# Optimization experiments

Hardware: AMD Instinct MI355X
Metric: run time of the kernel (lower is better)

## Reference

```python
import jax, jax.numpy as jnp
import numpy as np

N_NODES = 65536
N_EDGES = 1048576
IN_F = 128
HID_F = 128
OUT_F = 128


def setup_inputs() -> dict:
    key = jax.random.key(0)
    ks = jax.random.split(key, 8)
    feat = jax.random.normal(ks[0], (N_NODES, IN_F), dtype=jnp.float32)
    eweight = jax.random.uniform(ks[1], (N_EDGES, 1), dtype=jnp.float32)
    W1 = jax.random.normal(ks[2], (IN_F, HID_F), dtype=jnp.float32) * (1.0 / np.sqrt(IN_F))
    b1 = jnp.zeros((HID_F,), dtype=jnp.float32)
    W2 = jax.random.normal(ks[3], (HID_F, OUT_F), dtype=jnp.float32) * (1.0 / np.sqrt(HID_F))
    b2 = jnp.zeros((OUT_F,), dtype=jnp.float32)
    src = jax.random.randint(ks[4], (N_EDGES,), 0, N_NODES, dtype=jnp.int32)
    dst = jax.random.randint(ks[5], (N_EDGES,), 0, N_NODES, dtype=jnp.int32)
    return {"feat": feat, "eweight": eweight, "W1": W1, "b1": b1,
            "W2": W2, "b2": b2, "src": src, "dst": dst}


def _degrees(src, dst, n_nodes):
    ones = jnp.ones(src.shape[0], dtype=jnp.float32)
    deg_out = jax.ops.segment_sum(ones, src, num_segments=n_nodes)
    deg_in = jax.ops.segment_sum(ones, dst, num_segments=n_nodes)
    # DGL GraphConv clamps degree to min 1 before norm='both'
    return jnp.clip(deg_out, 1.0, None), jnp.clip(deg_in, 1.0, None)


def _graph_conv(feat, W, b, src, dst, out_norm, in_norm, n_nodes):
    # DGL GraphConv, norm='both': D_out^{-1/2} x -> x W -> spmm sum -> D_in^{-1/2} -> + b
    h = feat * out_norm[:, None]
    h = h @ W
    agg = jax.ops.segment_sum(h[src], dst, num_segments=n_nodes)
    return agg * in_norm[:, None] + b


def reference(feat, eweight, W1, b1, W2, b2, src, dst):
    n = feat.shape[0]
    deg_out, deg_in = _degrees(src, dst, n)
    out_norm = jax.lax.rsqrt(deg_out)
    in_norm = jax.lax.rsqrt(deg_in)
    h = _graph_conv(feat, W1, b1, src, dst, out_norm, in_norm, n)
    h = jax.nn.relu(h)
    h = _graph_conv(h, W2, b2, src, dst, out_norm, in_norm, n)
    # final update_all: u_mul_e + sum (eweight given)
    msg = h[src] * eweight  # [E, OUT_F]
    return jax.ops.segment_sum(msg, dst, num_segments=n)
```

## Files before the change

kernel.cpp:

```cpp
#include <hip/hip_runtime.h>

#define F 128
#define NBA 512
#define NBS 128
#define COARSE 256
#define CAP_BIN 4864
#define CAP_CSR 5632

typedef unsigned int uint;
typedef unsigned short ushort;
typedef unsigned char uchar;
typedef __attribute__((ext_vector_type(8))) short short8;
typedef __attribute__((ext_vector_type(8))) unsigned short ushort8;
typedef __attribute__((ext_vector_type(4))) float floatx4;

__device__ __forceinline__ ushort f2bf(float f) {
  uint u = __float_as_uint(f);
  u += 0x7fffu + ((u >> 16) & 1u);
  return (ushort)(u >> 16);
}

__global__ __launch_bounds__(256) void w_prep(const float* __restrict__ W1,
                                              const float* __restrict__ W2,
                                              ushort* __restrict__ W1t,
                                              ushort* __restrict__ W2t,
                                              int* __restrict__ cursorD,
                                              int* __restrict__ cursorS) {
  int b = blockIdx.x;
  if (b == 0) cursorD[threadIdx.x] = 0;
  if (b == 1) cursorS[threadIdx.x] = 0;
  const float* W = (b < 64) ? W1 : W2;
  ushort* Wt = (b < 64) ? W1t : W2t;
  int idx = (b & 63) * 256 + threadIdx.x;
  int k = idx >> 7, n = idx & 127;
  Wt[n * F + k] = f2bf(W[idx]);
}

__global__ __launch_bounds__(256) void bin_edges(
    const int* __restrict__ src, const int* __restrict__ dst,
    const float* __restrict__ ew, int E,
    int* __restrict__ cursorD, int* __restrict__ cursorS,
    uint2* __restrict__ slotD, uchar* __restrict__ srcF) {
  __shared__ int cnt[4][COARSE];
  __shared__ int base[COARSE];
  bool isD = blockIdx.x < NBA;
  int blk = isD ? blockIdx.x : blockIdx.x - NBA;
  int nblk = isD ? NBA : NBS;
  const int* key = isD ? dst : src;
  int* cursor = isD ? cursorD : cursorS;
  int wave = threadIdx.x >> 6;
  for (int i = threadIdx.x; i < 4 * COARSE; i += 256) ((int*)cnt)[i] = 0;
  __syncthreads();
  int chunk = (E + nblk - 1) / nblk;
  int s0 = blk * chunk, s1 = min(E, s0 + chunk);
  for (int i = s0 + threadIdx.x; i < s1; i += 256)
    atomicAdd(&cnt[wave][key[i] >> 8], 1);
  __syncthreads();
  if (threadIdx.x < COARSE) {
    int b = threadIdx.x;
    int tot = cnt[0][b] + cnt[1][b] + cnt[2][b] + cnt[3][b];
    base[b] = tot ? atomicAdd(&cursor[b], tot) : 0;
    cnt[0][b] = 0;
  }
  __syncthreads();
  if (isD) {
    for (int i = s0 + threadIdx.x; i < s1; i += 256) {
      int d = dst[i];
      int bin = d >> 8;
      int p = base[bin] + atomicAdd(&cnt[0][bin], 1);
      if (p < CAP_BIN) {
        uint2 v;
        v.x = (uint)(src[i] & 0xffff) | ((uint)f2bf(ew[i]) << 16);
        v.y = (uint)(d & 255);
        slotD[(size_t)bin * CAP_BIN + p] = v;
      }
    }
  } else {
    for (int i = s0 + threadIdx.x; i < s1; i += 256) {
      int s = src[i];
      int bin = s >> 8;
      int p = base[bin] + atomicAdd(&cnt[0][bin], 1);
      if (p < CAP_BIN) srcF[(size_t)bin * CAP_BIN + p] = (uchar)(s & 255);
    }
  }
}

__global__ __launch_bounds__(1024) void bucket_csr(
    const uint2* __restrict__ slotD, const int* __restrict__ cursorD,
    int2* __restrict__ rowRange, float* __restrict__ inNorm, uint* __restrict__ csr,
    const uchar* __restrict__ srcF, const int* __restrict__ cursorS,
    float* __restrict__ outNorm) {
  __shared__ int hist[256], base[256], cur[256];
  int t = threadIdx.x;
  if (blockIdx.x >= COARSE) {
    int b = blockIdx.x - COARSE;
    int lo = b * CAP_BIN;
    int cntS = min(cursorS[b], CAP_BIN);
    if (t < 256) hist[t] = 0;
    __syncthreads();
    for (int i = lo + t; i < lo + cntS; i += 1024)
      atomicAdd(&hist[srcF[i]], 1);
    __syncthreads();
    if (t < 256) outNorm[b * 256 + t] = rsqrtf((float)max(hist[t], 1));
    return;
  }
  int b = blockIdx.x;
  int lo = b * CAP_BIN;
  int cntD = min(cursorD[b], CAP_BIN);
  int hi = lo + cntD;
  if (t < 256) hist[t] = 0;
  __syncthreads();
  for (int i = lo + t; i < hi; i += 1024)
    atomicAdd(&hist[slotD[i].y], 1);
  __syncthreads();
  if (t < 256) base[t] = (hist[t] + 3) & ~3;
  __syncthreads();
  for (int off = 1; off < 256; off <<= 1) {
    int x = 0;
    if (t < 256 && t >= off) x = base[t - off];
    __syncthreads();
    if (t < 256) base[t] += x;
    __syncthreads();
  }
  if (t < 256) {
    int v = hist[t];
    int sz4 = (v + 3) & ~3;
    int st = b * CAP_CSR + base[t] - sz4;
    base[t] = st;
    cur[t] = 0;
    int node = b * 256 + t;
    rowRange[node] = make_int2(st, v);
    inNorm[node] = rsqrtf((float)max(v, 1));
    for (int p = st + v; p < st + sz4; ++p) csr[p] = 0x80000000u;
  }
  __syncthreads();
  for (int i = lo + t; i < hi; i += 1024) {
    uint2 v = slotD[i];
    int fine = v.y;
    int p = base[fine] + atomicAdd(&cur[fine], 1);
    csr[p] = v.x;
  }
}

template <bool BF16IN>
__global__ __launch_bounds__(256) void gemm_mfma(
    const void* __restrict__ Xv, const float* __restrict__ scale,
    const ushort* __restrict__ Wt, ushort* __restrict__ Y) {
  __shared__ ushort sA[128 * 136];
  __shared__ ushort sB[128 * 136];
  int t = threadIdx.x;
  int row0 = blockIdx.x * 128;

  {
    int r = t >> 1, hf = t & 1;
    ushort* ap = sA + r * 136 + hf * 64;
    if (BF16IN) {
      const ushort* xp = (const ushort*)Xv + (size_t)(row0 + r) * F + hf * 64;
#pragma unroll
      for (int j = 0; j < 8; ++j)
        *(ushort8*)(ap + j * 8) = *(const ushort8*)(xp + j * 8);
    } else {
      const float* xp = (const float*)Xv + (size_t)(row0 + r) * F + hf * 64;
      float s = scale[row0 + r];
#pragma unroll
      for (int j = 0; j < 8; ++j) {
        float4 v0 = *(const float4*)(xp + j * 8);
        float4 v1 = *(const float4*)(xp + j * 8 + 4);
        ushort8 o;
        o[0] = f2bf(v0.x * s); o[1] = f2bf(v0.y * s); o[2] = f2bf(v0.z * s); o[3] = f2bf(v0.w * s);
        o[4] = f2bf(v1.x * s); o[5] = f2bf(v1.y * s); o[6] = f2bf(v1.z * s); o[7] = f2bf(v1.w * s);
        *(ushort8*)(ap + j * 8) = o;
      }
    }
  }
  {
    int n = t >> 1, hf = t & 1;
    const ushort* wp = Wt + n * F + hf * 64;
    ushort* bp = sB + n * 136 + hf * 64;
#pragma unroll
    for (int j = 0; j < 8; ++j)
      *(ushort8*)(bp + j * 8) = *(const ushort8*)(wp + j * 8);
  }
  __syncthreads();

  int lane = t & 63, wave = t >> 6;
  int quad = lane >> 4, l16 = lane & 15;
  int mrow0 = wave * 32;

  floatx4 acc[2][8];
#pragma unroll
  for (int a = 0; a < 2; ++a)
#pragma unroll
    for (int c = 0; c < 8; ++c) acc[a][c] = (floatx4){0.f, 0.f, 0.f, 0.f};

#pragma unroll
  for (int kc = 0; kc < 128; kc += 32) {
    short8 afrag[2], bfrag[8];
#pragma unroll
    for (int a = 0; a < 2; ++a)
      afrag[a] = *(const short8*)(sA + (mrow0 + a * 16 + l16) * 136 + kc + quad * 8);
#pragma unroll
    for (int c = 0; c < 8; ++c)
      bfrag[c] = *(const short8*)(sB + (c * 16 + l16) * 136 + kc + quad * 8);
#pragma unroll
    for (int a = 0; a < 2; ++a)
#pragma unroll
      for (int c = 0; c < 8; ++c)
        acc[a][c] = __builtin_amdgcn_mfma_f32_16x16x32_bf16(afrag[a], bfrag[c], acc[a][c], 0, 0, 0);
  }

#pragma unroll
  for (int a = 0; a < 2; ++a)
#pragma unroll
    for (int c = 0; c < 8; ++c)
#pragma unroll
      for (int r = 0; r < 4; ++r) {
        int row = row0 + mrow0 + a * 16 + quad * 4 + r;
        int col = c * 16 + l16;
        Y[(size_t)row * F + col] = f2bf(acc[a][c][r]);
      }
}


template <bool EW, bool NB, bool RELU, bool PS, bool OUT_BF16>
__global__ __launch_bounds__(256) void spmm(
    const ushort* __restrict__ hb, const int2* __restrict__ rowRange,
    const uint* __restrict__ csr, const float* __restrict__ inNorm,
    const float* __restrict__ bias, const float* __restrict__ postScale,
    void* __restrict__ outv) {
  int lane = threadIdx.x & 63;
  int g = lane >> 4;
  int j = lane & 15;
  int n = blockIdx.x * 4 + (threadIdx.x >> 6);
  int2 r = rowRange[n];
  int len4 = (r.y + 3) & ~3;
  const char* hbB = (const char*)hb;
  uint joff = (uint)j << 4;
  float acc[8] = {0.f, 0.f, 0.f, 0.f, 0.f, 0.f, 0.f, 0.f};

#define GQ(e, c, q)                                                      \
  {                                                                      \
    uint ei = (e);                                                       \
    c = *(const uint4*)(hbB + (((ei & 0xffffu) << 8) | joff));           \
    q = EW ? __uint_as_float(ei & 0xffff0000u)                           \
           : ((int)ei >= 0 ? 1.0f : 0.0f);                               \
  }
#define ACC8(c, q)                                                      \
  {                                                                     \
    acc[0] = fmaf(__uint_as_float(c.x << 16), q, acc[0]);               \
    acc[1] = fmaf(__uint_as_float(c.x & 0xffff0000u), q, acc[1]);       \
    acc[2] = fmaf(__uint_as_float(c.y << 16), q, acc[2]);               \
    acc[3] = fmaf(__uint_as_float(c.y & 0xffff0000u), q, acc[3]);       \
    acc[4] = fmaf(__uint_as_float(c.z << 16), q, acc[4]);               \
    acc[5] = fmaf(__uint_as_float(c.z & 0xffff0000u), q, acc[5]);       \
    acc[6] = fmaf(__uint_as_float(c.w << 16), q, acc[6]);               \
    acc[7] = fmaf(__uint_as_float(c.w & 0xffff0000u), q, acc[7]);       \
  }

  int i = 0;
  for (; i + 16 <= len4; i += 16) {
    uint4 ee = *(const uint4*)(csr + r.x + i + 4 * g);
    uint4 c0, c1, c2, c3;
    float q0, q1, q2, q3;
    GQ(ee.x, c0, q0) GQ(ee.y, c1, q1) GQ(ee.z, c2, q2) GQ(ee.w, c3, q3)
    ACC8(c0, q0) ACC8(c1, q1) ACC8(c2, q2) ACC8(c3, q3)
  }
  if (i + 8 <= len4) {
    uint2 ee = *(const uint2*)(csr + r.x + i + 2 * g);
    uint4 c0, c1;
    float q0, q1;
    GQ(ee.x, c0, q0) GQ(ee.y, c1, q1)
    ACC8(c0, q0) ACC8(c1, q1)
    i += 8;
  }
  if (i < len4) {
    uint e = csr[r.x + i + g];
    uint4 c0;
    float q0;
    GQ(e, c0, q0)
    ACC8(c0, q0)
  }
#undef GQ
#undef ACC8

#pragma unroll
  for (int k = 0; k < 8; ++k) {
    acc[k] += __shfl_xor(acc[k], 16, 64);
    acc[k] += __shfl_xor(acc[k], 32, 64);
  }
  if (g != 0) return;

  if (NB) {
    float sc = inNorm[n];
    float4 b0 = ((const float4*)bias)[2 * j];
    float4 b1 = ((const float4*)bias)[2 * j + 1];
    float bb[8] = {b0.x, b0.y, b0.z, b0.w, b1.x, b1.y, b1.z, b1.w};
#pragma unroll
    for (int k = 0; k < 8; ++k) {
      acc[k] = fmaf(acc[k], sc, bb[k]);
      if (RELU) acc[k] = fmaxf(acc[k], 0.f);
    }
    if (PS) {
      float o = postScale[n];
#pragma unroll
      for (int k = 0; k < 8; ++k) acc[k] *= o;
    }
  }
  if (OUT_BF16) {
    uint4 o;
    o.x = ((uint)f2bf(acc[1]) << 16) | (uint)f2bf(acc[0]);
    o.y = ((uint)f2bf(acc[3]) << 16) | (uint)f2bf(acc[2]);
    o.z = ((uint)f2bf(acc[5]) << 16) | (uint)f2bf(acc[4]);
    o.w = ((uint)f2bf(acc[7]) << 16) | (uint)f2bf(acc[6]);
    ((uint4*)outv)[(size_t)n * 16 + j] = o;
  } else {
    float4 lo = {acc[0], acc[1], acc[2], acc[3]};
    float4 hi = {acc[4], acc[5], acc[6], acc[7]};
    ((float4*)outv)[(size_t)n * 32 + 2 * j] = lo;
    ((float4*)outv)[(size_t)n * 32 + 2 * j + 1] = hi;
  }
}


extern "C" void kernel_launch(void* const* d_in, const int* in_sizes, int n_in,
                              void* d_out, int out_size, void* d_ws, size_t ws_size,
                              hipStream_t stream) {
  const float* feat = (const float*)d_in[0];
  const float* ew   = (const float*)d_in[1];
  const float* W1   = (const float*)d_in[2];
  const float* b1   = (const float*)d_in[3];
  const float* W2   = (const float*)d_in[4];
  const float* b2   = (const float*)d_in[5];
  const int*   src  = (const int*)d_in[6];
  const int*   dst  = (const int*)d_in[7];
  const int N = in_sizes[0] / F;
  const int E = in_sizes[6];
  float* out = (float*)d_out;

  char* ws = (char*)d_ws;
  size_t off = 0;
  auto alloc = [&](size_t bytes) {
    void* p = ws + off;
    off += (bytes + 255) & ~(size_t)255;
    return p;
  };
  int2*   rowRange = (int2*)alloc((size_t)N * 8);
  float*  inNorm   = (float*)alloc((size_t)N * 4);
  float*  outNorm  = (float*)alloc((size_t)N * 4);
  ushort* W1t      = (ushort*)alloc((size_t)F * F * 2);
  ushort* W2t      = (ushort*)alloc((size_t)F * F * 2);
  int*    cursorD  = (int*)alloc(COARSE * 4);
  int*    cursorS  = (int*)alloc(COARSE * 4);
  uint*   csr      = (uint*)alloc((size_t)COARSE * CAP_CSR * 4);
  ushort* bufAb    = (ushort*)alloc((size_t)N * F * 2);
  ushort* bufBb    = (ushort*)alloc((size_t)N * F * 2);
  ushort* bufCb    = (ushort*)alloc((size_t)N * F * 2);
  if (off > ws_size) return;

  uint2* slotD;
  uchar* srcF;
  {
    char* tp = (char*)bufBb;
    size_t toff = 0;
    auto talloc = [&](size_t bytes) {
      void* p = tp + toff;
      toff += (bytes + 255) & ~(size_t)255;
      return p;
    };
    slotD = (uint2*)talloc((size_t)COARSE * CAP_BIN * 8);
    srcF  = (uchar*)talloc((size_t)COARSE * CAP_BIN);
  }

  w_prep<<<128, 256, 0, stream>>>(W1, W2, W1t, W2t, cursorD, cursorS);
  bin_edges<<<NBA + NBS, 256, 0, stream>>>(src, dst, ew, E, cursorD, cursorS, slotD, srcF);
  bucket_csr<<<2 * COARSE, 1024, 0, stream>>>(slotD, cursorD, rowRange, inNorm, csr,
                                              srcF, cursorS, outNorm);

  gemm_mfma<false><<<N / 128, 256, 0, stream>>>(feat, outNorm, W1t, bufAb);
  spmm<false, true, true, true, true><<<N / 4, 256, 0, stream>>>(
      bufAb, rowRange, csr, inNorm, b1, outNorm, bufBb);
  gemm_mfma<true><<<N / 128, 256, 0, stream>>>(bufBb, nullptr, W2t, bufAb);
  spmm<false, true, false, false, true><<<N / 4, 256, 0, stream>>>(
      bufAb, rowRange, csr, inNorm, b2, nullptr, bufCb);
  spmm<true, false, false, false, false><<<N / 4, 256, 0, stream>>>(
      bufCb, rowRange, csr, nullptr, nullptr, nullptr, out);
}
```

Before: 273.8 us.

## Map one 16-lane group per node in SpMM instead of one wavefront

The SpMM kernels now assign each 16-lane quarter-wavefront its own destination node, so a 256-thread block handles 16 nodes instead of 4. Each group walks its full edge list 8 edges at a time, and the cross-group shuffle reduction is removed. This removes the reduction and the idle lanes on the write-out, and puts more loads in flight per thread. In exchange, the four groups in a wavefront now have different degrees and diverge, and each thread holds more registers for its 8 gathered rows.

```diff
diff --git a/kernel.cpp b/kernel.cpp
--- a/kernel.cpp
+++ b/kernel.cpp
@@ -231,7 +231,7 @@
   int lane = threadIdx.x & 63;
   int g = lane >> 4;
   int j = lane & 15;
-  int n = blockIdx.x * 4 + (threadIdx.x >> 6);
+  int n = blockIdx.x * 16 + (threadIdx.x >> 6) * 4 + g;
   int2 r = rowRange[n];
   int len4 = (r.y + 3) & ~3;
   const char* hbB = (const char*)hb;
@@ -258,37 +258,26 @@
   }
 
   int i = 0;
-  for (; i + 16 <= len4; i += 16) {
-    uint4 ee = *(const uint4*)(csr + r.x + i + 4 * g);
+  while (i + 8 <= len4) {
+    uint4 e0 = *(const uint4*)(csr + r.x + i);
+    uint4 e1 = *(const uint4*)(csr + r.x + i + 4);
+    uint4 c0, c1, c2, c3, c4, c5, c6, c7;
+    float q0, q1, q2, q3, q4, q5, q6, q7;
+    GQ(e0.x, c0, q0) GQ(e0.y, c1, q1) GQ(e0.z, c2, q2) GQ(e0.w, c3, q3)
+    GQ(e1.x, c4, q4) GQ(e1.y, c5, q5) GQ(e1.z, c6, q6) GQ(e1.w, c7, q7)
+    ACC8(c0, q0) ACC8(c1, q1) ACC8(c2, q2) ACC8(c3, q3)
+    ACC8(c4, q4) ACC8(c5, q5) ACC8(c6, q6) ACC8(c7, q7)
+    i += 8;
+  }
+  if (i < len4) {
+    uint4 e0 = *(const uint4*)(csr + r.x + i);
     uint4 c0, c1, c2, c3;
     float q0, q1, q2, q3;
-    GQ(ee.x, c0, q0) GQ(ee.y, c1, q1) GQ(ee.z, c2, q2) GQ(ee.w, c3, q3)
+    GQ(e0.x, c0, q0) GQ(e0.y, c1, q1) GQ(e0.z, c2, q2) GQ(e0.w, c3, q3)
     ACC8(c0, q0) ACC8(c1, q1) ACC8(c2, q2) ACC8(c3, q3)
-  }
-  if (i + 8 <= len4) {
-    uint2 ee = *(const uint2*)(csr + r.x + i + 2 * g);
-    uint4 c0, c1;
-    float q0, q1;
-    GQ(ee.x, c0, q0) GQ(ee.y, c1, q1)
-    ACC8(c0, q0) ACC8(c1, q1)
-    i += 8;
-  }
-  if (i < len4) {
-    uint e = csr[r.x + i + g];
-    uint4 c0;
-    float q0;
-    GQ(e, c0, q0)
-    ACC8(c0, q0)
   }
 #undef GQ
 #undef ACC8
-
-#pragma unroll
-  for (int k = 0; k < 8; ++k) {
-    acc[k] += __shfl_xor(acc[k], 16, 64);
-    acc[k] += __shfl_xor(acc[k], 32, 64);
-  }
-  if (g != 0) return;
 
   if (NB) {
     float sc = inNorm[n];
@@ -377,11 +366,11 @@
                                               srcF, cursorS, outNorm);
 
   gemm_mfma<false><<<N / 128, 256, 0, stream>>>(feat, outNorm, W1t, bufAb);
-  spmm<false, true, true, true, true><<<N / 4, 256, 0, stream>>>(
+  spmm<false, true, true, true, true><<<N / 16, 256, 0, stream>>>(
       bufAb, rowRange, csr, inNorm, b1, outNorm, bufBb);
   gemm_mfma<true><<<N / 128, 256, 0, stream>>>(bufBb, nullptr, W2t, bufAb);
-  spmm<false, true, false, false, true><<<N / 4, 256, 0, stream>>>(
+  spmm<false, true, false, false, true><<<N / 16, 256, 0, stream>>>(
       bufAb, rowRange, csr, inNorm, b2, nullptr, bufCb);
-  spmm<true, false, false, false, false><<<N / 4, 256, 0, stream>>>(
+  spmm<true, false, false, false, false><<<N / 16, 256, 0, stream>>>(
       bufCb, rowRange, csr, nullptr, nullptr, nullptr, out);
 }
```

After: 269.3 us. Within noise of the previous version (-1.6%).
